# Kernel tuning notes

Measured on AMD Instinct MI355X. Metric: run time of the kernel, lower is better.

The kernel has to match this reference:

```python
import jax, jax.numpy as jnp
import numpy as np
from jax import lax

N, T, D_IN = 8192, 64, 64
R = 256            # reservoir_dim
K = 3              # diffusion hops
D_OUT = 64
E = 131072
LEAK = 0.3
SPECTRAL_RADIUS = 0.9
SPARSITY = 0.9


def setup_inputs() -> dict:
    key = jax.random.key(0)
    kx, ke = jax.random.split(key)
    rng = np.random.default_rng(0)

    # ESN fixed buffers (match torch init: randn*0.1; sparse randn scaled to rho)
    W_in = (rng.standard_normal((R, D_IN)) * 0.1).astype(np.float32)
    W_res = rng.standard_normal((R, R)).astype(np.float32)
    mask = rng.random((R, R)) < SPARSITY
    W_res[mask] = 0.0
    rho = float(np.abs(np.linalg.eigvals(W_res)).max())
    if rho > 1e-8:
        W_res = W_res * (SPECTRAL_RADIUS / rho)

    # readout: Linear((K+1)*R -> 2*D_OUT), GELU, Linear(2*D_OUT -> D_OUT), LayerNorm
    fan1 = (K + 1) * R
    W1 = (rng.standard_normal((2 * D_OUT, fan1)) / np.sqrt(fan1)).astype(np.float32)
    b1 = np.zeros((2 * D_OUT,), np.float32)
    W2 = (rng.standard_normal((D_OUT, 2 * D_OUT)) / np.sqrt(2 * D_OUT)).astype(np.float32)
    b2 = np.zeros((D_OUT,), np.float32)
    gamma = np.ones((D_OUT,), np.float32)
    beta = np.zeros((D_OUT,), np.float32)

    x = jax.random.normal(kx, (N, T, D_IN), dtype=jnp.float32)
    edge_index = jax.random.randint(ke, (2, E), 0, N, dtype=jnp.int64)

    return {
        "x": x,
        "edge_index": edge_index,
        "W_in": jnp.asarray(W_in),
        "W_res": jnp.asarray(W_res),
        "W1": jnp.asarray(W1), "b1": jnp.asarray(b1),
        "W2": jnp.asarray(W2), "b2": jnp.asarray(b2),
        "gamma": jnp.asarray(gamma), "beta": jnp.asarray(beta),
    }


def _esn(x, W_in, W_res):
    # x: [N, T, D_IN] -> final reservoir state [N, R]
    x_proj = jnp.einsum("ntd,rd->tnr", x, W_in)  # [T, N, R]

    def step(h, xp_t):
        h_new = jnp.tanh(xp_t + h @ W_res.T)
        return (1.0 - LEAK) * h + LEAK * h_new, None

    h0 = jnp.zeros((x.shape[0], W_res.shape[0]), dtype=x.dtype)
    h, _ = lax.scan(step, h0, x_proj)
    return h


def _norm_adj(edge_index, n_nodes):
    # symmetric D^{-1/2} A D^{-1/2}; dedup handled by idempotent .set
    row = jnp.concatenate([edge_index[0], edge_index[1]])
    col = jnp.concatenate([edge_index[1], edge_index[0]])
    A_bin = jnp.zeros((n_nodes, n_nodes), jnp.float32).at[row, col].set(1.0)
    deg = A_bin.sum(axis=1)
    dinv = jnp.where(deg > 0, 1.0 / jnp.sqrt(jnp.maximum(deg, 1e-12)), 0.0)
    dinv = jnp.minimum(dinv, 1e6)
    return dinv[:, None] * A_bin * dinv[None, :]


def reference(x, edge_index, W_in, W_res, W1, b1, W2, b2, gamma, beta):
    h = _esn(x, W_in, W_res)                    # [N, R]
    A = _norm_adj(edge_index, x.shape[0])       # [N, N]

    diffused = [h]
    h_k = h
    for _ in range(K):
        h_k = A @ h_k
        diffused.append(h_k)
    cat = jnp.concatenate(diffused, axis=-1)    # [N, (K+1)*R]

    z = jax.nn.gelu(cat @ W1.T + b1, approximate=False)
    z = z @ W2.T + b2                           # [N, D_OUT]
    mu = z.mean(axis=-1, keepdims=True)
    var = z.var(axis=-1, keepdims=True)
    z = (z - mu) / jnp.sqrt(var + 1e-5)
    return z * gamma + beta
```

## Files before the change

### kernel.cpp

```cpp
#include <hip/hip_runtime.h>
#include <hip/hip_bf16.h>
#include <hip/hip_fp16.h>
#include <math.h>

#define NN    8192
#define TT    64
#define DIN   64
#define RR    256
#define DOUT  64
#define HID   128
#define CATD  1024
#define NE    131072
#define MASKW 256
#define MAXD  256
#define HROW  328
#define C8ROW 768

typedef __attribute__((ext_vector_type(8))) short    s16x8;
typedef __attribute__((ext_vector_type(8))) _Float16 f16x8;
typedef __attribute__((ext_vector_type(4))) float    f32x4;
typedef __attribute__((ext_vector_type(2))) float    f32x2;

static __device__ __forceinline__ unsigned short f2bs(float f) {
  union { __hip_bfloat16 b; unsigned short u; } cv;
  cv.b = __float2bfloat16(f);
  return cv.u;
}
static __device__ __forceinline__ unsigned int pack2bf(float a, float b) {
  return (unsigned int)f2bs(a) | ((unsigned int)f2bs(b) << 16);
}
static __device__ __forceinline__ unsigned int pack2h(float a, float b) {
  return (unsigned int)__half_as_ushort(__float2half(a))
       | ((unsigned int)__half_as_ushort(__float2half(b)) << 16);
}
static __device__ __forceinline__ unsigned int pack4fp8(float a, float b, float c, float d) {
  unsigned int p = 0;
  p = __builtin_amdgcn_cvt_pk_fp8_f32(a, b, (int)p, false);
  p = __builtin_amdgcn_cvt_pk_fp8_f32(c, d, (int)p, true);
  return p;
}


__global__ __launch_bounds__(256) void setup_kernel(
    uint4* __restrict__ mask4,
    const float* __restrict__ Wres, const float* __restrict__ Win,
    const float* __restrict__ W1, const float* __restrict__ W2,
    unsigned short* __restrict__ wresh, unsigned short* __restrict__ winh,
    unsigned short* __restrict__ W1h, unsigned short* __restrict__ W2h) {
  int i = blockIdx.x * 256 + threadIdx.x;
  mask4[i] = make_uint4(0u, 0u, 0u, 0u);
  if (i < 65536) wresh[i] = f2bs(Wres[i]);
  else if (i < 81920) winh[i - 65536] = f2bs(Win[i - 65536]);
  else if (i < 212992) W1h[i - 81920] = __half_as_ushort(__float2half(W1[i - 81920]));
  else if (i < 221184) W2h[i - 212992] = __half_as_ushort(__float2half(W2[i - 212992]));
}

__global__ __launch_bounds__(256) void edge_kernel(const int* __restrict__ eidx,
                                                   unsigned int* __restrict__ mask) {
  int e = blockIdx.x * 256 + threadIdx.x;
  if (e < NE) {
    int u = eidx[e];
    int v = eidx[NE + e];
    atomicOr(&mask[(size_t)u * MASKW + (v >> 5)], 1u << (v & 31));
    atomicOr(&mask[(size_t)v * MASKW + (u >> 5)], 1u << (u & 31));
  }
}

__global__ __launch_bounds__(256) void nbrlist_kernel(const unsigned int* __restrict__ mask,
                                                      unsigned short* __restrict__ nbrlist,
                                                      int* __restrict__ nbrcnt,
                                                      float* __restrict__ dinv) {
  __shared__ int wsum[4];
  const int n = blockIdx.x;
  const int tid = threadIdx.x;
  const int lane = tid & 63;
  const int w = tid >> 6;
  unsigned int m = mask[(size_t)n * MASKW + tid];
  const int c = __popc(m);
  int inc = c;
#pragma unroll
  for (int d = 1; d < 64; d <<= 1) {
    int v = __shfl_up(inc, d, 64);
    if (lane >= d) inc += v;
  }
  if (lane == 63) wsum[w] = inc;
  __syncthreads();
  int base = 0;
  for (int i = 0; i < w; ++i) base += wsum[i];
  int off = base + inc - c;
  while (m) {
    int b = __ffs(m) - 1;
    m &= m - 1;
    if (off < MAXD) nbrlist[(size_t)n * MAXD + off] = (unsigned short)(tid * 32 + b);
    ++off;
  }
  if (tid == 255) {
    int tot = base + inc;
    nbrcnt[n] = tot < MAXD ? tot : MAXD;
    dinv[n] = (tot > 0) ? fminf(rsqrtf((float)tot), 1e6f) : 0.0f;
  }
}

__global__ __launch_bounds__(512, 4) void esn_mfma_kernel(
    const float* __restrict__ x,
    const unsigned short* __restrict__ winh,
    const unsigned short* __restrict__ wresh,
    unsigned short* __restrict__ cat,
    unsigned char* __restrict__ cat8)
{
  __shared__ unsigned short hs[2][16][HROW];
  const int tid  = threadIdx.x;
  const int lane = tid & 63;
  const int w    = tid >> 6;
  const int lr   = lane & 15;
  const int lg   = lane >> 4;
  const int sn   = tid >> 5;
  const int sq   = tid & 31;
  const long gn0 = (long)blockIdx.x * 16;
  const int bx   = (lr >> 3) & 1;
  const int lgx  = lg ^ bx;
  const int lgw  = (lg >> 1) ^ bx;
  const int bs   = (sn >> 3) & 1;

  s16x8 waug[2][10];
#pragma unroll
  for (int rt = 0; rt < 2; ++rt) {
    const int r = w * 32 + rt * 16 + lr;
#pragma unroll
    for (int kt = 0; kt < 8; ++kt)
      waug[rt][kt] = *(const s16x8*)(wresh + r * RR + kt * 32 + lg * 8);
#pragma unroll
    for (int kt = 8; kt < 10; ++kt)
      waug[rt][kt] = *(const s16x8*)(winh + r * DIN + (kt - 8) * 32 + lg * 8);
  }

  unsigned short* const rd0 = &hs[0][0][0] + lr * HROW + lgx * 8;
  unsigned short* const rd1 = &hs[1][0][0] + lr * HROW + lgx * 8;
  unsigned short* const wh0 = &hs[0][0][0] + lr * HROW + (w * 4 + lgw) * 8 + (lg & 1) * 4;
  unsigned short* const wh1 = &hs[1][0][0] + lr * HROW + (w * 4 + lgw) * 8 + (lg & 1) * 4;
  unsigned short* const xs0 = &hs[0][0][0] + sn * HROW + (32 + ((sq >> 2) ^ bs)) * 8 + (sq & 3) * 2;
  unsigned short* const xs1 = &hs[1][0][0] + sn * HROW + (32 + ((sq >> 2) ^ bs)) * 8 + (sq & 3) * 2;

  for (int i = tid; i < 16 * HROW / 2; i += 512) ((unsigned int*)hs[0])[i] = 0u;

  const float* xrow = x + (gn0 + sn) * (long)(TT * DIN) + sq * 2;
  float2 xr0 = *(const float2*)(xrow);
  float2 xr1 = *(const float2*)(xrow + DIN);
  __syncthreads();
  *(unsigned int*)xs0 = pack2bf(xr0.x, xr0.y);
  xr0 = *(const float2*)(xrow + 2 * DIN);

  f32x4 hreg[2];
  hreg[0] = (f32x4){0.f, 0.f, 0.f, 0.f};
  hreg[1] = (f32x4){0.f, 0.f, 0.f, 0.f};
  __syncthreads();

#define ESN_STEP(RD, WH, XS, XRS, XRL, TNEXT)                                        \
  {                                                                                  \
    f32x4 a0e = (f32x4){0.f,0.f,0.f,0.f}, a0o = a0e, a1e = a0e, a1o = a0e;           \
    __builtin_amdgcn_s_setprio(1);                                                   \
    _Pragma("unroll")                                                                \
    for (int kt = 0; kt < 10; kt += 2) {                                             \
      const s16x8 hbe = *(const s16x8*)(RD + kt * 32);                               \
      const s16x8 hbo = *(const s16x8*)(RD + (kt + 1) * 32);                         \
      a0e = __builtin_amdgcn_mfma_f32_16x16x32_bf16(waug[0][kt], hbe, a0e, 0, 0, 0); \
      a1e = __builtin_amdgcn_mfma_f32_16x16x32_bf16(waug[1][kt], hbe, a1e, 0, 0, 0); \
      a0o = __builtin_amdgcn_mfma_f32_16x16x32_bf16(waug[0][kt+1], hbo, a0o, 0, 0, 0);\
      a1o = __builtin_amdgcn_mfma_f32_16x16x32_bf16(waug[1][kt+1], hbo, a1o, 0, 0, 0);\
    }                                                                                \
    __builtin_amdgcn_s_setprio(0);                                                   \
    *(unsigned int*)(XS) = pack2bf(XRS.x, XRS.y);                 \
    XRL = *(const float2*)(xrow + (TNEXT) * DIN);                      \
    _Pragma("unroll")                                                                \
    for (int rt = 0; rt < 2; ++rt) {                                                 \
      const f32x4 ae = rt ? a1e : a0e;                                               \
      const f32x4 ao = rt ? a1o : a0o;                                               \
      f32x4 hn;                                                                      \
      _Pragma("unroll")                                                              \
      for (int i = 0; i < 4; ++i) {                                                  \
        const float sacc = ae[i] + ao[i];                                            \
        const float e = __builtin_amdgcn_exp2f(sacc * 2.8853900817779268f);          \
        const float rc = __builtin_amdgcn_rcpf(e + 1.0f);                            \
        hn[i] = fmaf(-0.6f, rc, fmaf(0.7f, hreg[rt][i], 0.3f));                      \
      }                                                                              \
      hreg[rt] = hn;                                                                 \
      *(uint2*)(WH + rt * 16) =                                                      \
          make_uint2(pack2bf(hn[0], hn[1]), pack2bf(hn[2], hn[3]));                  \
    }                                                                                \
  }

  for (int tc = 0; tc < TT / 2; ++tc) {
    const int t = tc * 2;
    const int tla = (t + 3 < TT) ? t + 3 : TT - 1;
    ESN_STEP(rd0, wh1, xs1, xr1, xr1, tla);
    __syncthreads();
    const int tlb = (t + 4 < TT) ? t + 4 : TT - 1;
    ESN_STEP(rd1, wh0, xs0, xr0, xr0, tlb);
    __syncthreads();
  }
#undef ESN_STEP

#pragma unroll
  for (int rt = 0; rt < 2; ++rt) {
    *(uint2*)(cat + (gn0 + lr) * CATD + w * 32 + rt * 16 + lg * 4) =
        make_uint2(pack2h(hreg[rt][0], hreg[rt][1]), pack2h(hreg[rt][2], hreg[rt][3]));
    *(unsigned int*)(cat8 + (gn0 + lr) * C8ROW + w * 32 + rt * 16 + lg * 4) =
        pack4fp8(hreg[rt][0], hreg[rt][1], hreg[rt][2], hreg[rt][3]);
  }
}

__global__ __launch_bounds__(256) void spmv_kernel(
    const unsigned short* __restrict__ nbrlist, const int* __restrict__ nbrcnt,
    const float* __restrict__ dinv, unsigned short* __restrict__ cat,
    unsigned char* __restrict__ cat8, int hop)
{
  const int wv   = threadIdx.x >> 6;
  const int lane = threadIdx.x & 63;
  const int half = lane >> 5;
  const int li   = lane & 31;
  const int n    = blockIdx.x * 8 + wv * 2 + half;
  const int cnt  = nbrcnt[n];
  const unsigned char* in8 = cat8 + (size_t)(hop - 1) * RR;
  float acc[8];
#pragma unroll
  for (int k = 0; k < 8; ++k) acc[k] = 0.0f;

  for (int c0 = 0; c0 < cnt; c0 += 32) {
    const int m = (cnt - c0 < 32) ? cnt - c0 : 32;
    int idx = 0; float dv = 0.f;
    if (li < m) {
      idx = (int)nbrlist[(size_t)n * MAXD + c0 + li];
      dv  = dinv[idx];
    }
#pragma unroll 8
    for (int i = 0; i < m; ++i) {
      const int   j  = __shfl(idx, half * 32 + i, 64);
      const float wj = __shfl(dv,  half * 32 + i, 64);
      const uint2 u  = *(const uint2*)(in8 + (size_t)j * C8ROW + li * 8);
      const f32x2 f0 = __builtin_amdgcn_cvt_pk_f32_fp8((int)u.x, false);
      const f32x2 f1 = __builtin_amdgcn_cvt_pk_f32_fp8((int)u.x, true);
      const f32x2 f2 = __builtin_amdgcn_cvt_pk_f32_fp8((int)u.y, false);
      const f32x2 f3 = __builtin_amdgcn_cvt_pk_f32_fp8((int)u.y, true);
      acc[0] += wj * f0[0]; acc[1] += wj * f0[1];
      acc[2] += wj * f1[0]; acc[3] += wj * f1[1];
      acc[4] += wj * f2[0]; acc[5] += wj * f2[1];
      acc[6] += wj * f3[0]; acc[7] += wj * f3[1];
    }
  }
  const float dn = dinv[n];
#pragma unroll
  for (int k = 0; k < 8; ++k) acc[k] *= dn;
  uint4 o;
  o.x = pack2h(acc[0], acc[1]);
  o.y = pack2h(acc[2], acc[3]);
  o.z = pack2h(acc[4], acc[5]);
  o.w = pack2h(acc[6], acc[7]);
  *(uint4*)(cat + (size_t)n * CATD + (size_t)hop * RR + li * 8) = o;
  if (hop < 3) {
    uint2 o8;
    o8.x = pack4fp8(acc[0], acc[1], acc[2], acc[3]);
    o8.y = pack4fp8(acc[4], acc[5], acc[6], acc[7]);
    *(uint2*)(cat8 + (size_t)n * C8ROW + (size_t)hop * RR + li * 8) = o8;
  }
}

__global__ __launch_bounds__(256) void readout_kernel(
    const unsigned short* __restrict__ cat,
    const unsigned short* __restrict__ W1h,
    const float* __restrict__ b1,
    const unsigned short* __restrict__ W2h,
    const float* __restrict__ b2, const float* __restrict__ gamma,
    const float* __restrict__ beta, float* __restrict__ out)
{
  __shared__ unsigned short z1[32][136];
  __shared__ float z2[32][68];
  const int tid  = threadIdx.x;
  const int lane = tid & 63;
  const int w    = tid >> 6;
  const int lr   = lane & 15;
  const int lg   = lane >> 4;
  const long gn0 = (long)blockIdx.x * 32;

  f32x4 a00 = (f32x4){0.f,0.f,0.f,0.f}, a01 = a00, a10 = a00, a11 = a00;
  const unsigned short* arow0 = cat + (gn0 + lr) * CATD;
  const unsigned short* arow1 = cat + (gn0 + 16 + lr) * CATD;
  const unsigned short* brow0 = W1h + (w * 32 + lr) * CATD;
  const unsigned short* brow1 = W1h + (w * 32 + 16 + lr) * CATD;
#pragma unroll 8
  for (int kt = 0; kt < 32; ++kt) {
    const f16x8 af0 = *(const f16x8*)(arow0 + kt * 32 + lg * 8);
    const f16x8 af1 = *(const f16x8*)(arow1 + kt * 32 + lg * 8);
    const f16x8 bf0 = *(const f16x8*)(brow0 + kt * 32 + lg * 8);
    const f16x8 bf1 = *(const f16x8*)(brow1 + kt * 32 + lg * 8);
    a00 = __builtin_amdgcn_mfma_f32_16x16x32_f16(af0, bf0, a00, 0, 0, 0);
    a01 = __builtin_amdgcn_mfma_f32_16x16x32_f16(af0, bf1, a01, 0, 0, 0);
    a10 = __builtin_amdgcn_mfma_f32_16x16x32_f16(af1, bf0, a10, 0, 0, 0);
    a11 = __builtin_amdgcn_mfma_f32_16x16x32_f16(af1, bf1, a11, 0, 0, 0);
  }
  const float is2 = 0.70710678118654752f;
#pragma unroll
  for (int nt = 0; nt < 2; ++nt) {
#pragma unroll
    for (int ht = 0; ht < 2; ++ht) {
      const int hid = w * 32 + ht * 16 + lr;
      const float bb = b1[hid];
      const f32x4 a = nt ? (ht ? a11 : a10) : (ht ? a01 : a00);
#pragma unroll
      for (int i = 0; i < 4; ++i) {
        const float v = a[i] + bb;
        const float g = 0.5f * v * (1.0f + erff(v * is2));
        z1[nt * 16 + lg * 4 + i][hid] = __half_as_ushort(__float2half(g));
      }
    }
  }
  __syncthreads();

  f32x4 c20 = (f32x4){0.f,0.f,0.f,0.f}, c21 = c20;
  const unsigned short* w2row = W2h + (w * 16 + lr) * HID;
#pragma unroll
  for (int kt = 0; kt < 4; ++kt) {
    const f16x8 bf  = *(const f16x8*)(w2row + kt * 32 + lg * 8);
    const f16x8 af0 = *(const f16x8*)(&z1[lr][kt * 32 + lg * 8]);
    const f16x8 af1 = *(const f16x8*)(&z1[16 + lr][kt * 32 + lg * 8]);
    c20 = __builtin_amdgcn_mfma_f32_16x16x32_f16(af0, bf, c20, 0, 0, 0);
    c21 = __builtin_amdgcn_mfma_f32_16x16x32_f16(af1, bf, c21, 0, 0, 0);
  }
  {
    const float bb = b2[w * 16 + lr];
#pragma unroll
    for (int i = 0; i < 4; ++i) {
      z2[lg * 4 + i][w * 16 + lr]      = c20[i] + bb;
      z2[16 + lg * 4 + i][w * 16 + lr] = c21[i] + bb;
    }
  }
  __syncthreads();

  {
    const int n = tid >> 3;
    const int c = tid & 7;
    float v[8], s = 0.0f, s2 = 0.0f;
#pragma unroll
    for (int k2 = 0; k2 < 8; ++k2) {
      v[k2] = z2[n][c + 8 * k2];
      s += v[k2]; s2 += v[k2] * v[k2];
    }
#pragma unroll
    for (int m = 1; m < 8; m <<= 1) {
      s  += __shfl_xor(s,  m, 64);
      s2 += __shfl_xor(s2, m, 64);
    }
    const float mu  = s * (1.0f / 64.0f);
    const float var = s2 * (1.0f / 64.0f) - mu * mu;
    const float inv = rsqrtf(var + 1e-5f);
    float* orow = out + (gn0 + n) * DOUT;
#pragma unroll
    for (int k2 = 0; k2 < 8; ++k2)
      orow[c + 8 * k2] = (v[k2] - mu) * inv * gamma[c + 8 * k2] + beta[c + 8 * k2];
  }
}


extern "C" void kernel_launch(void* const* d_in, const int* in_sizes, int n_in,
                              void* d_out, int out_size, void* d_ws, size_t ws_size,
                              hipStream_t stream) {
  const float* x     = (const float*)d_in[0];
  const int*   eidx  = (const int*)d_in[1];
  const float* W_in  = (const float*)d_in[2];
  const float* W_res = (const float*)d_in[3];
  const float* W1    = (const float*)d_in[4];
  const float* b1    = (const float*)d_in[5];
  const float* W2    = (const float*)d_in[6];
  const float* b2    = (const float*)d_in[7];
  const float* gamma = (const float*)d_in[8];
  const float* beta  = (const float*)d_in[9];
  float* out = (float*)d_out;

  char* ws = (char*)d_ws;
  size_t off = 0;
  auto alloc = [&](size_t bytes) {
    void* p = ws + off;
    off += (bytes + 255) & ~(size_t)255;
    return p;
  };
  unsigned int*   mask    = (unsigned int*)  alloc((size_t)NN * MASKW * 4);
  unsigned short* cat     = (unsigned short*)alloc((size_t)NN * CATD * 2);
  unsigned char*  cat8    = (unsigned char*) alloc((size_t)NN * C8ROW);
  unsigned short* nbrlist = (unsigned short*)alloc((size_t)NN * MAXD * 2);
  int*            nbrcnt  = (int*)           alloc((size_t)NN * 4);
  float*          dinv    = (float*)         alloc((size_t)NN * 4);
  unsigned short* wresh   = (unsigned short*)alloc((size_t)RR * RR * 2);
  unsigned short* winh    = (unsigned short*)alloc((size_t)RR * DIN * 2);
  unsigned short* W1h     = (unsigned short*)alloc((size_t)HID * CATD * 2);
  unsigned short* W2h     = (unsigned short*)alloc((size_t)DOUT * HID * 2);

  setup_kernel<<<2048, 256, 0, stream>>>((uint4*)mask, W_res, W_in, W1, W2,
                                         wresh, winh, W1h, W2h);
  edge_kernel<<<NE / 256, 256, 0, stream>>>(eidx, mask);
  nbrlist_kernel<<<NN, 256, 0, stream>>>(mask, nbrlist, nbrcnt, dinv);

  esn_mfma_kernel<<<NN / 16, 512, 0, stream>>>(x, winh, wresh, cat, cat8);

  for (int k = 1; k <= 3; ++k)
    spmv_kernel<<<NN / 8, 256, 0, stream>>>(nbrlist, nbrcnt, dinv, cat, cat8, k);

  readout_kernel<<<NN / 32, 256, 0, stream>>>(cat, W1h, b1, W2h, b2, gamma, beta, out);
}
```

Before: 188.0 us.

## Merge ESN accumulator chains and double readout waves per block

The ESN step now accumulates into a single chain per output tile instead of splitting even and odd k-tiles into two chains, which removes the final add but serialises the MFMA dependency chain. The readout kernel moves from 256 to 512 threads per block. Each of the 8 waves now computes one 16-column hidden tile instead of two, the second GEMM is split across all 8 waves, and the LayerNorm is spread over 16 threads per row. This raises parallelism in the readout at the cost of more redundant A-operand loads per block, and it may lengthen the latency-bound ESN recurrence.

```diff
diff --git a/kernel.cpp b/kernel.cpp
--- a/kernel.cpp
+++ b/kernel.cpp
@@ -157,29 +157,24 @@
 
 #define ESN_STEP(RD, WH, XS, XRS, XRL, TNEXT)                                        \
   {                                                                                  \
-    f32x4 a0e = (f32x4){0.f,0.f,0.f,0.f}, a0o = a0e, a1e = a0e, a1o = a0e;           \
+    f32x4 a0 = (f32x4){0.f,0.f,0.f,0.f}, a1 = a0;                                    \
     __builtin_amdgcn_s_setprio(1);                                                   \
     _Pragma("unroll")                                                                \
-    for (int kt = 0; kt < 10; kt += 2) {                                             \
-      const s16x8 hbe = *(const s16x8*)(RD + kt * 32);                               \
-      const s16x8 hbo = *(const s16x8*)(RD + (kt + 1) * 32);                         \
-      a0e = __builtin_amdgcn_mfma_f32_16x16x32_bf16(waug[0][kt], hbe, a0e, 0, 0, 0); \
-      a1e = __builtin_amdgcn_mfma_f32_16x16x32_bf16(waug[1][kt], hbe, a1e, 0, 0, 0); \
-      a0o = __builtin_amdgcn_mfma_f32_16x16x32_bf16(waug[0][kt+1], hbo, a0o, 0, 0, 0);\
-      a1o = __builtin_amdgcn_mfma_f32_16x16x32_bf16(waug[1][kt+1], hbo, a1o, 0, 0, 0);\
+    for (int kt = 0; kt < 10; ++kt) {                                                \
+      const s16x8 hb = *(const s16x8*)(RD + kt * 32);                                \
+      a0 = __builtin_amdgcn_mfma_f32_16x16x32_bf16(waug[0][kt], hb, a0, 0, 0, 0);    \
+      a1 = __builtin_amdgcn_mfma_f32_16x16x32_bf16(waug[1][kt], hb, a1, 0, 0, 0);    \
     }                                                                                \
     __builtin_amdgcn_s_setprio(0);                                                   \
     *(unsigned int*)(XS) = pack2bf(XRS.x, XRS.y);                 \
     XRL = *(const float2*)(xrow + (TNEXT) * DIN);                      \
     _Pragma("unroll")                                                                \
     for (int rt = 0; rt < 2; ++rt) {                                                 \
-      const f32x4 ae = rt ? a1e : a0e;                                               \
-      const f32x4 ao = rt ? a1o : a0o;                                               \
+      const f32x4 ae = rt ? a1 : a0;                                                 \
       f32x4 hn;                                                                      \
       _Pragma("unroll")                                                              \
       for (int i = 0; i < 4; ++i) {                                                  \
-        const float sacc = ae[i] + ao[i];                                            \
-        const float e = __builtin_amdgcn_exp2f(sacc * 2.8853900817779268f);          \
+        const float e = __builtin_amdgcn_exp2f(ae[i] * 2.8853900817779268f);         \
         const float rc = __builtin_amdgcn_rcpf(e + 1.0f);                            \
         hn[i] = fmaf(-0.6f, rc, fmaf(0.7f, hreg[rt][i], 0.3f));                      \
       }                                                                              \
@@ -264,7 +259,7 @@
   }
 }
 
-__global__ __launch_bounds__(256) void readout_kernel(
+__global__ __launch_bounds__(512) void readout_kernel(
     const unsigned short* __restrict__ cat,
     const unsigned short* __restrict__ W1h,
     const float* __restrict__ b1,
@@ -281,30 +276,25 @@
   const int lg   = lane >> 4;
   const long gn0 = (long)blockIdx.x * 32;
 
-  f32x4 a00 = (f32x4){0.f,0.f,0.f,0.f}, a01 = a00, a10 = a00, a11 = a00;
+  f32x4 a0 = (f32x4){0.f,0.f,0.f,0.f}, a1 = a0;
   const unsigned short* arow0 = cat + (gn0 + lr) * CATD;
   const unsigned short* arow1 = cat + (gn0 + 16 + lr) * CATD;
-  const unsigned short* brow0 = W1h + (w * 32 + lr) * CATD;
-  const unsigned short* brow1 = W1h + (w * 32 + 16 + lr) * CATD;
+  const unsigned short* brow  = W1h + (w * 16 + lr) * CATD;
 #pragma unroll 8
   for (int kt = 0; kt < 32; ++kt) {
     const f16x8 af0 = *(const f16x8*)(arow0 + kt * 32 + lg * 8);
     const f16x8 af1 = *(const f16x8*)(arow1 + kt * 32 + lg * 8);
-    const f16x8 bf0 = *(const f16x8*)(brow0 + kt * 32 + lg * 8);
-    const f16x8 bf1 = *(const f16x8*)(brow1 + kt * 32 + lg * 8);
-    a00 = __builtin_amdgcn_mfma_f32_16x16x32_f16(af0, bf0, a00, 0, 0, 0);
-    a01 = __builtin_amdgcn_mfma_f32_16x16x32_f16(af0, bf1, a01, 0, 0, 0);
-    a10 = __builtin_amdgcn_mfma_f32_16x16x32_f16(af1, bf0, a10, 0, 0, 0);
-    a11 = __builtin_amdgcn_mfma_f32_16x16x32_f16(af1, bf1, a11, 0, 0, 0);
+    const f16x8 bf  = *(const f16x8*)(brow  + kt * 32 + lg * 8);
+    a0 = __builtin_amdgcn_mfma_f32_16x16x32_f16(af0, bf, a0, 0, 0, 0);
+    a1 = __builtin_amdgcn_mfma_f32_16x16x32_f16(af1, bf, a1, 0, 0, 0);
   }
   const float is2 = 0.70710678118654752f;
-#pragma unroll
-  for (int nt = 0; nt < 2; ++nt) {
-#pragma unroll
-    for (int ht = 0; ht < 2; ++ht) {
-      const int hid = w * 32 + ht * 16 + lr;
-      const float bb = b1[hid];
-      const f32x4 a = nt ? (ht ? a11 : a10) : (ht ? a01 : a00);
+  {
+    const int hid = w * 16 + lr;
+    const float bb = b1[hid];
+#pragma unroll
+    for (int nt = 0; nt < 2; ++nt) {
+      const f32x4 a = nt ? a1 : a0;
 #pragma unroll
       for (int i = 0; i < 4; ++i) {
         const float v = a[i] + bb;
@@ -315,37 +305,34 @@
   }
   __syncthreads();
 
-  f32x4 c20 = (f32x4){0.f,0.f,0.f,0.f}, c21 = c20;
-  const unsigned short* w2row = W2h + (w * 16 + lr) * HID;
-#pragma unroll
-  for (int kt = 0; kt < 4; ++kt) {
-    const f16x8 bf  = *(const f16x8*)(w2row + kt * 32 + lg * 8);
-    const f16x8 af0 = *(const f16x8*)(&z1[lr][kt * 32 + lg * 8]);
-    const f16x8 af1 = *(const f16x8*)(&z1[16 + lr][kt * 32 + lg * 8]);
-    c20 = __builtin_amdgcn_mfma_f32_16x16x32_f16(af0, bf, c20, 0, 0, 0);
-    c21 = __builtin_amdgcn_mfma_f32_16x16x32_f16(af1, bf, c21, 0, 0, 0);
-  }
   {
-    const float bb = b2[w * 16 + lr];
-#pragma unroll
-    for (int i = 0; i < 4; ++i) {
-      z2[lg * 4 + i][w * 16 + lr]      = c20[i] + bb;
-      z2[16 + lg * 4 + i][w * 16 + lr] = c21[i] + bb;
-    }
+    const int nt = w >> 2;
+    const int ot = w & 3;
+    f32x4 c2 = (f32x4){0.f,0.f,0.f,0.f};
+    const unsigned short* w2row = W2h + (ot * 16 + lr) * HID;
+#pragma unroll
+    for (int kt = 0; kt < 4; ++kt) {
+      const f16x8 af = *(const f16x8*)(&z1[nt * 16 + lr][kt * 32 + lg * 8]);
+      const f16x8 bf = *(const f16x8*)(w2row + kt * 32 + lg * 8);
+      c2 = __builtin_amdgcn_mfma_f32_16x16x32_f16(af, bf, c2, 0, 0, 0);
+    }
+    const float bb = b2[ot * 16 + lr];
+#pragma unroll
+    for (int i = 0; i < 4; ++i) z2[nt * 16 + lg * 4 + i][ot * 16 + lr] = c2[i] + bb;
   }
   __syncthreads();
 
   {
-    const int n = tid >> 3;
-    const int c = tid & 7;
-    float v[8], s = 0.0f, s2 = 0.0f;
-#pragma unroll
-    for (int k2 = 0; k2 < 8; ++k2) {
-      v[k2] = z2[n][c + 8 * k2];
+    const int n = tid >> 4;
+    const int c = tid & 15;
+    float v[4], s = 0.0f, s2 = 0.0f;
+#pragma unroll
+    for (int k2 = 0; k2 < 4; ++k2) {
+      v[k2] = z2[n][c + 16 * k2];
       s += v[k2]; s2 += v[k2] * v[k2];
     }
 #pragma unroll
-    for (int m = 1; m < 8; m <<= 1) {
+    for (int m = 1; m < 16; m <<= 1) {
       s  += __shfl_xor(s,  m, 64);
       s2 += __shfl_xor(s2, m, 64);
     }
@@ -354,8 +341,8 @@
     const float inv = rsqrtf(var + 1e-5f);
     float* orow = out + (gn0 + n) * DOUT;
 #pragma unroll
-    for (int k2 = 0; k2 < 8; ++k2)
-      orow[c + 8 * k2] = (v[k2] - mu) * inv * gamma[c + 8 * k2] + beta[c + 8 * k2];
+    for (int k2 = 0; k2 < 4; ++k2)
+      orow[c + 16 * k2] = (v[k2] - mu) * inv * gamma[c + 16 * k2] + beta[c + 16 * k2];
   }
 }
 
@@ -403,5 +390,5 @@
   for (int k = 1; k <= 3; ++k)
     spmv_kernel<<<NN / 8, 256, 0, stream>>>(nbrlist, nbrcnt, dinv, cat, cat8, k);
 
-  readout_kernel<<<NN / 32, 256, 0, stream>>>(cat, W1h, b1, W2h, b2, gamma, beta, out);
-}
+  readout_kernel<<<NN / 32, 512, 0, stream>>>(cat, W1h, b1, W2h, b2, gamma, beta, out);
+}
```

Result: no change. 187.8 us (-0.1%).
